# Kernel optimization log

Hardware: AMD Instinct MI355X
Metric: run time of the kernel (lower is better)

The kernel has to match this reference:

```python
import jax, jax.numpy as jnp
import numpy as np

B, S, F, DV, H, DH, L = 32, 600, 9, 1024, 16, 64, 2


def setup_inputs() -> dict:
    key = jax.random.key(0)
    ks = jax.random.split(key, 24)
    w = lambda k, shape, s=0.05: jax.random.normal(k, shape, dtype=jnp.float32) * s
    return {
        "x": w(ks[0], (B, S, F), 1.0),
        "enc_in_W": w(ks[1], (F, DV)), "enc_in_b": w(ks[2], (DV,)),
        "Wq": w(ks[3], (L, H, DV, DH)), "bq": w(ks[4], (L, H, DH)),
        "Wk": w(ks[5], (L, H, DV, DH)), "bk": w(ks[6], (L, H, DH)),
        "Wv": w(ks[7], (L, H, DV, DH)), "bv": w(ks[8], (L, H, DH)),
        "Wo": w(ks[9], (L, DV, DV)), "bo": w(ks[10], (L, DV)),
        "W1": w(ks[11], (L, DV, DV)), "b1": w(ks[12], (L, DV)),
        "W2": w(ks[13], (L, DV, DV)), "b2": w(ks[14], (L, DV)),
        "ln1_w": jnp.ones((L, DV)), "ln1_b": jnp.zeros((L, DV)),
        "ln2_w": jnp.ones((L, DV)), "ln2_b": jnp.zeros((L, DV)),
        "out_W": w(ks[15], (DV, F)), "out_b": w(ks[16], (F,)),
    }


def _layernorm(v, g, b):
    mu = v.mean(-1, keepdims=True)
    var = v.var(-1, keepdims=True)  # biased, matches torch LayerNorm
    return (v - mu) / jnp.sqrt(var + 1e-5) * g + b


def reference(x, enc_in_W, enc_in_b, Wq, bq, Wk, bk, Wv, bv, Wo, bo,
              W1, b1, W2, b2, ln1_w, ln1_b, ln2_w, ln2_b, out_W, out_b):
    # enc_input_fc; pe skipped (code checks pe_mode == 'stardard', never true)
    h = x @ enc_in_W + enc_in_b  # [B,S,DV]
    scale = 1.0 / jnp.sqrt(jnp.float32(DH))
    for l in range(L):
        q = jnp.einsum('bsd,hdk->bhsk', h, Wq[l]) + bq[l][None, :, None, :]
        k = jnp.einsum('bsd,hdk->bhsk', h, Wk[l]) + bk[l][None, :, None, :]
        v = jnp.einsum('bsd,hdk->bhsk', h, Wv[l]) + bv[l][None, :, None, :]
        attn = jax.nn.softmax(jnp.einsum('bhsk,bhtk->bhst', q, k) * scale, axis=-1)
        ctx = jnp.einsum('bhst,bhtk->bhsk', attn, v)  # [B,H,S,DH]
        # torch: stack(heads, dim=-1) -> [B,S,DH,H], then flatten(start_dim=2)
        a = ctx.transpose(0, 2, 3, 1).reshape(B, S, DH * H)
        attn_out = a @ Wo[l] + bo[l]
        x1 = _layernorm(h + attn_out, ln1_w[l], ln1_b[l])
        ff = jax.nn.elu(x1 @ W2[l] + b2[l]) @ W1[l] + b1[l]  # fc1(elu(fc2(x1)))
        h = _layernorm(x1 + ff, ln2_w[l], ln2_b[l])
    out = h @ out_W + out_b  # [B,S,F]; in_seq_len == out_seq_len -> no out_seq_fc
    return out
```

## Files before the change

### kernel.cpp

```cpp
#include <hip/hip_runtime.h>

typedef unsigned short u16;
typedef unsigned int u32;
typedef __attribute__((ext_vector_type(8))) short shortx8;
typedef __attribute__((ext_vector_type(4))) float floatx4;
typedef __attribute__((ext_vector_type(4))) u32 uintx4;
typedef __attribute__((ext_vector_type(2))) u32 uintx2;

#define AS1 __attribute__((address_space(1)))
#define AS3 __attribute__((address_space(3)))

__device__ __forceinline__ float bf2f(u16 u) {
  return __builtin_bit_cast(float, ((u32)u) << 16);
}
__device__ __forceinline__ u16 f2bf(float f) {
  u32 i = __builtin_bit_cast(u32, f);
  u32 r = (i + 0x7fffu + ((i >> 16) & 1u)) >> 16;
  return (u16)r;
}

__launch_bounds__(256)
__global__ void pack_qkv_t(const float* __restrict__ W, u16* __restrict__ dst) {
  __shared__ u16 T[64][72];
  const int kt = blockIdx.x, y = blockIdx.y;
  const int l = y >> 4, h = y & 15;
  const int t = threadIdx.x;
  const int rr = t >> 2, cq = (t & 3) * 16;
  const float* src = W + ((size_t)y * 1024 + kt * 64 + rr) * 64 + cq;
#pragma unroll
  for (int e4 = 0; e4 < 4; ++e4) {
    float4 f = *(const float4*)(src + e4 * 4);
    T[cq + e4 * 4 + 0][rr] = f2bf(f.x);
    T[cq + e4 * 4 + 1][rr] = f2bf(f.y);
    T[cq + e4 * 4 + 2][rr] = f2bf(f.z);
    T[cq + e4 * 4 + 3][rr] = f2bf(f.w);
  }
  __syncthreads();
  const int dd = t >> 2, kq = (t & 3) * 16;
  u16* drow = dst + (size_t)l * 3145728 + ((size_t)h * 64 + dd) * 1024 + kt * 64 + kq;
  *(uintx4*)(drow) = *(const uintx4*)&T[dd][kq];
  *(uintx4*)(drow + 8) = *(const uintx4*)&T[dd][kq + 8];
}

__launch_bounds__(256)
__global__ void pack_sq_t(const float* __restrict__ W, u16* __restrict__ dst) {
  __shared__ u16 T[64][72];
  const int ct = blockIdx.x & 15, rt = blockIdx.x >> 4, l = blockIdx.y;
  const int t = threadIdx.x;
  const int rr = t >> 2, cq = (t & 3) * 16;
  const float* src = W + (size_t)l * 1048576 + (size_t)(rt * 64 + rr) * 1024 + ct * 64 + cq;
#pragma unroll
  for (int e4 = 0; e4 < 4; ++e4) {
    float4 f = *(const float4*)(src + e4 * 4);
    T[cq + e4 * 4 + 0][rr] = f2bf(f.x);
    T[cq + e4 * 4 + 1][rr] = f2bf(f.y);
    T[cq + e4 * 4 + 2][rr] = f2bf(f.z);
    T[cq + e4 * 4 + 3][rr] = f2bf(f.w);
  }
  __syncthreads();
  const int cc = t >> 2, rq = (t & 3) * 16;
  u16* drow = dst + (size_t)l * 1048576 + (size_t)(ct * 64 + cc) * 1024 + rt * 64 + rq;
  *(uintx4*)(drow) = *(const uintx4*)&T[cc][rq];
  *(uintx4*)(drow + 8) = *(const uintx4*)&T[cc][rq + 8];
}

__launch_bounds__(256)
__global__ void pack_wo_t(const float* __restrict__ W, u16* __restrict__ dst) {
  __shared__ u16 T[64][72];
  const int rt = blockIdx.x >> 4, nt = blockIdx.x & 15, l = blockIdx.y;
  const int t = threadIdx.x;
  const int rr = t >> 2, cq = (t & 3) * 16;
  const float* src = W + (size_t)l * 1048576 + (size_t)(rt * 64 + rr) * 1024 + nt * 64 + cq;
#pragma unroll
  for (int e4 = 0; e4 < 4; ++e4) {
    float4 f = *(const float4*)(src + e4 * 4);
    T[cq + e4 * 4 + 0][rr] = f2bf(f.x);
    T[cq + e4 * 4 + 1][rr] = f2bf(f.y);
    T[cq + e4 * 4 + 2][rr] = f2bf(f.z);
    T[cq + e4 * 4 + 3][rr] = f2bf(f.w);
  }
  __syncthreads();
  const int hh = t & 15;
#pragma unroll
  for (int pass = 0; pass < 4; ++pass) {
    const int nl = pass * 16 + (t >> 4);
    uintx2 pk;
    u16 v0 = T[nl][0 * 16 + hh], v1 = T[nl][1 * 16 + hh];
    u16 v2 = T[nl][2 * 16 + hh], v3 = T[nl][3 * 16 + hh];
    pk[0] = (u32)v0 | ((u32)v1 << 16);
    pk[1] = (u32)v2 | ((u32)v3 << 16);
    *(uintx2*)&dst[(size_t)l * 1048576 + (size_t)(nt * 64 + nl) * 1024 + hh * 64 + rt * 4] = pk;
  }
}

__launch_bounds__(256)
__global__ void pack_bias(const float* __restrict__ bq, const float* __restrict__ bk,
                          const float* __restrict__ bv, float* __restrict__ bias) {
  const int i = blockIdx.x * 256 + threadIdx.x;
  const int l = i / 3072, n = i % 3072;
  const int which = n >> 10, nn = n & 1023;
  const float* s = (which == 0) ? bq : (which == 1) ? bk : bv;
  bias[i] = s[l * 1024 + nn];
}

__launch_bounds__(256)
__global__ void enc_kernel(const float* __restrict__ x, const float* __restrict__ W,
                           const float* __restrict__ bias, u16* __restrict__ h) {
  const size_t i = (size_t)blockIdx.x * 256 + threadIdx.x;
  const int m = (int)(i >> 10), n = (int)(i & 1023);
  const float* xr = x + (size_t)m * 9;
  float acc = bias[n];
#pragma unroll
  for (int f = 0; f < 9; ++f) acc += xr[f] * W[f * 1024 + n];
  h[i] = f2bf(acc);
}

template <int EPI>
__launch_bounds__(256)
__global__ void gemm_bt(const u16* __restrict__ A, int lda,
                        const u16* __restrict__ Bt,
                        const float* __restrict__ bias,
                        const u16* __restrict__ R, int ldr,
                        u16* __restrict__ C, int ldc) {
  constexpr int K = 1024;
  __shared__ u16 As[128 * 64];
  __shared__ u16 Bs[128 * 64];
  const int tid = threadIdx.x;
  const int lane = tid & 63;
  const int w = tid >> 6;
  const int wr = w >> 1, wc = w & 1;
  const int m0 = blockIdx.y * 128, n0 = blockIdx.x * 128;

  floatx4 acc[4][4];
#pragma unroll
  for (int i = 0; i < 4; ++i)
#pragma unroll
    for (int j = 0; j < 4; ++j) acc[i][j] = (floatx4){0.f, 0.f, 0.f, 0.f};

  const u16* Ab = A + (size_t)m0 * lda;
  const u16* Bb = Bt + (size_t)n0 * K;

  for (int k0 = 0; k0 < K; k0 += 64) {
#pragma unroll
    for (int p = 0; p < 4; ++p) {
      const int o = p * 4096 + tid * 16;
      const int row = o >> 7;
      const int ke = (o & 127) >> 1;
      __builtin_amdgcn_global_load_lds((const AS1 void*)(Ab + (size_t)row * lda + (k0 + ke)),
                                       (AS3 void*)((char*)As + o), 16, 0, 0);
      __builtin_amdgcn_global_load_lds((const AS1 void*)(Bb + (size_t)row * K + (k0 + ke)),
                                       (AS3 void*)((char*)Bs + o), 16, 0, 0);
    }
    __syncthreads();
#pragma unroll
    for (int ks = 0; ks < 2; ++ks) {
      shortx8 af[4], bfr[4];
#pragma unroll
      for (int i = 0; i < 4; ++i) {
        const int ar = wr * 64 + i * 16 + (lane & 15);
        af[i] = *(const shortx8*)&As[ar * 64 + ks * 32 + (lane >> 4) * 8];
        const int br = wc * 64 + i * 16 + (lane & 15);
        bfr[i] = *(const shortx8*)&Bs[br * 64 + ks * 32 + (lane >> 4) * 8];
      }
#pragma unroll
      for (int i = 0; i < 4; ++i)
#pragma unroll
        for (int j = 0; j < 4; ++j)
          acc[i][j] = __builtin_amdgcn_mfma_f32_16x16x32_bf16(af[i], bfr[j], acc[i][j], 0, 0, 0);
    }
    __syncthreads();
  }

  const int lr = (lane >> 4) * 4, lc = lane & 15;
#pragma unroll
  for (int i = 0; i < 4; ++i) {
#pragma unroll
    for (int j = 0; j < 4; ++j) {
      const int col = n0 + wc * 64 + j * 16 + lc;
      const float bv = bias[col];
#pragma unroll
      for (int r = 0; r < 4; ++r) {
        const int row = m0 + wr * 64 + i * 16 + lr + r;
        float v = acc[i][j][r] + bv;
        if (EPI == 1) v += bf2f(R[(size_t)row * ldr + col]);
        if (EPI == 2) v = v > 0.f ? v : expm1f(v);
        C[(size_t)row * ldc + col] = f2bf(v);
      }
    }
  }
}

__launch_bounds__(512)
__global__ void gemm_bt_wide(const u16* __restrict__ A, int lda,
                             const u16* __restrict__ Bt,
                             const float* __restrict__ bias,
                             u16* __restrict__ C, int ldc) {
  constexpr int K = 1024;
  __shared__ u16 As[128 * 64];
  __shared__ u16 Bs[256 * 64];
  const int tid = threadIdx.x;
  const int lane = tid & 63;
  const int w = tid >> 6;
  const int wr = w >> 2, wc = w & 3;
  const int m0 = blockIdx.y * 128, n0 = blockIdx.x * 256;

  floatx4 acc[4][4];
#pragma unroll
  for (int i = 0; i < 4; ++i)
#pragma unroll
    for (int j = 0; j < 4; ++j) acc[i][j] = (floatx4){0.f, 0.f, 0.f, 0.f};

  const u16* Ab = A + (size_t)m0 * lda;
  const u16* Bb = Bt + (size_t)n0 * K;

  for (int k0 = 0; k0 < K; k0 += 64) {
#pragma unroll
    for (int p = 0; p < 2; ++p) {
      const int o = p * 8192 + tid * 16;
      const int row = o >> 7;
      const int ke = (o & 127) >> 1;
      __builtin_amdgcn_global_load_lds((const AS1 void*)(Ab + (size_t)row * lda + (k0 + ke)),
                                       (AS3 void*)((char*)As + o), 16, 0, 0);
    }
#pragma unroll
    for (int p = 0; p < 4; ++p) {
      const int o = p * 8192 + tid * 16;
      const int row = o >> 7;
      const int ke = (o & 127) >> 1;
      __builtin_amdgcn_global_load_lds((const AS1 void*)(Bb + (size_t)row * K + (k0 + ke)),
                                       (AS3 void*)((char*)Bs + o), 16, 0, 0);
    }
    __syncthreads();
#pragma unroll
    for (int ks = 0; ks < 2; ++ks) {
      shortx8 af[4], bfr[4];
#pragma unroll
      for (int i = 0; i < 4; ++i) {
        const int ar = wr * 64 + i * 16 + (lane & 15);
        af[i] = *(const shortx8*)&As[ar * 64 + ks * 32 + (lane >> 4) * 8];
        const int br = wc * 64 + i * 16 + (lane & 15);
        bfr[i] = *(const shortx8*)&Bs[br * 64 + ks * 32 + (lane >> 4) * 8];
      }
#pragma unroll
      for (int i = 0; i < 4; ++i)
#pragma unroll
        for (int j = 0; j < 4; ++j)
          acc[i][j] = __builtin_amdgcn_mfma_f32_16x16x32_bf16(af[i], bfr[j], acc[i][j], 0, 0, 0);
    }
    __syncthreads();
  }

  const int lr = (lane >> 4) * 4, lc = lane & 15;
#pragma unroll
  for (int i = 0; i < 4; ++i) {
#pragma unroll
    for (int j = 0; j < 4; ++j) {
      const int col = n0 + wc * 64 + j * 16 + lc;
      const float bv = bias[col];
#pragma unroll
      for (int r = 0; r < 4; ++r) {
        const int row = m0 + wr * 64 + i * 16 + lr + r;
        C[(size_t)row * ldc + col] = f2bf(acc[i][j][r] + bv);
      }
    }
  }
}

__launch_bounds__(256)
__global__ void attn_mfma(const u16* __restrict__ qkv, u16* __restrict__ aout) {
  const int qt = blockIdx.x, bh = blockIdx.y;
  const int b = bh >> 4, h = bh & 15;
  const int tid = threadIdx.x, lane = tid & 63, w = tid >> 6;
  const int g = lane >> 4, lq = lane & 15;

  __shared__ u16 K_ld[128 * 72];
  __shared__ u16 Vt[64 * 136];
  __shared__ u16 P_ld[4][16 * 136];

  const size_t bbase = (size_t)b * 600 * 3072;
  const int q0 = qt * 128 + w * 32;

  shortx8 aq[2][2];
#pragma unroll
  for (int sub = 0; sub < 2; ++sub) {
    const int s = q0 + sub * 16 + lq;
    if (s < 600) {
      const u16* qp = qkv + bbase + (size_t)s * 3072 + h * 64 + g * 8;
      aq[sub][0] = *(const shortx8*)qp;
      aq[sub][1] = *(const shortx8*)(qp + 32);
    } else {
      aq[sub][0] = (shortx8){0, 0, 0, 0, 0, 0, 0, 0};
      aq[sub][1] = (shortx8){0, 0, 0, 0, 0, 0, 0, 0};
    }
  }

  floatx4 Oa[2][4];
  float m[2][4], l[2][4];
#pragma unroll
  for (int sub = 0; sub < 2; ++sub) {
#pragma unroll
    for (int db = 0; db < 4; ++db) Oa[sub][db] = (floatx4){0.f, 0.f, 0.f, 0.f};
#pragma unroll
    for (int r = 0; r < 4; ++r) { m[sub][r] = -1e30f; l[sub][r] = 0.f; }
  }

  for (int ch = 0; ch < 5; ++ch) {
    const int t0 = ch * 128;
    __syncthreads();
    {
      const int tloc = tid >> 1, dhalf = (tid & 1) * 32;
      const int tg = t0 + tloc;
      if (tg < 600) {
        const u16* kp = qkv + bbase + (size_t)tg * 3072 + 1024 + h * 64 + dhalf;
        const u16* vp = kp + 1024;
#pragma unroll
        for (int c = 0; c < 4; ++c)
          *(uintx4*)&K_ld[tloc * 72 + dhalf + c * 8] = *(const uintx4*)(kp + c * 8);
#pragma unroll
        for (int c = 0; c < 4; ++c) {
          shortx8 vv = *(const shortx8*)(vp + c * 8);
#pragma unroll
          for (int e = 0; e < 8; ++e)
            Vt[(dhalf + c * 8 + e) * 136 + tloc] = (u16)vv[e];
        }
      } else {
        const uintx4 z4 = (uintx4){0, 0, 0, 0};
#pragma unroll
        for (int c = 0; c < 4; ++c)
          *(uintx4*)&K_ld[tloc * 72 + dhalf + c * 8] = z4;
#pragma unroll
        for (int c = 0; c < 4; ++c)
#pragma unroll
          for (int e = 0; e < 8; ++e)
            Vt[(dhalf + c * 8 + e) * 136 + tloc] = 0;
      }
    }
    __syncthreads();

#pragma unroll
    for (int sub = 0; sub < 2; ++sub) {
      floatx4 S[8];
#pragma unroll
      for (int jb = 0; jb < 8; ++jb) {
        S[jb] = (floatx4){0.f, 0.f, 0.f, 0.f};
#pragma unroll
        for (int ks = 0; ks < 2; ++ks) {
          shortx8 bk = *(const shortx8*)&K_ld[(jb * 16 + lq) * 72 + ks * 32 + g * 8];
          S[jb] = __builtin_amdgcn_mfma_f32_16x16x32_bf16(aq[sub][ks], bk, S[jb], 0, 0, 0);
        }
      }
#pragma unroll
      for (int jb = 0; jb < 8; ++jb) {
        const int tg = t0 + jb * 16 + lq;
        const bool ok = tg < 600;
#pragma unroll
        for (int r = 0; r < 4; ++r) S[jb][r] = ok ? S[jb][r] * 0.125f : -1e30f;
      }

      float scale[4];
#pragma unroll
      for (int r = 0; r < 4; ++r) {
        float v = S[0][r];
#pragma unroll
        for (int jb = 1; jb < 8; ++jb) v = fmaxf(v, S[jb][r]);
        v = fmaxf(v, __shfl_xor(v, 1));
        v = fmaxf(v, __shfl_xor(v, 2));
        v = fmaxf(v, __shfl_xor(v, 4));
        v = fmaxf(v, __shfl_xor(v, 8));
        const float mn = fmaxf(m[sub][r], v);
        scale[r] = __expf(m[sub][r] - mn);
        m[sub][r] = mn;
        l[sub][r] *= scale[r];
      }
#pragma unroll
      for (int db = 0; db < 4; ++db)
#pragma unroll
        for (int r = 0; r < 4; ++r) Oa[sub][db][r] *= scale[r];

      float sums[4] = {0.f, 0.f, 0.f, 0.f};
#pragma unroll
      for (int jb = 0; jb < 8; ++jb)
#pragma unroll
        for (int r = 0; r < 4; ++r) {
          const float p = __expf(S[jb][r] - m[sub][r]);
          sums[r] += p;
          P_ld[w][(g * 4 + r) * 136 + jb * 16 + lq] = f2bf(p);
        }
#pragma unroll
      for (int r = 0; r < 4; ++r) {
        float v = sums[r];
        v += __shfl_xor(v, 1);
        v += __shfl_xor(v, 2);
        v += __shfl_xor(v, 4);
        v += __shfl_xor(v, 8);
        l[sub][r] += v;
      }

#pragma unroll
      for (int ks = 0; ks < 4; ++ks) {
        shortx8 ap = *(const shortx8*)&P_ld[w][lq * 136 + ks * 32 + g * 8];
#pragma unroll
        for (int db = 0; db < 4; ++db) {
          shortx8 bv = *(const shortx8*)&Vt[(db * 16 + lq) * 136 + ks * 32 + g * 8];
          Oa[sub][db] = __builtin_amdgcn_mfma_f32_16x16x32_bf16(ap, bv, Oa[sub][db], 0, 0, 0);
        }
      }
    }
  }

#pragma unroll
  for (int sub = 0; sub < 2; ++sub) {
#pragma unroll
    for (int r = 0; r < 4; ++r) {
      const int sg = q0 + sub * 16 + g * 4 + r;
      if (sg < 600) {
        const float inv = 1.f / l[sub][r];
        u16* orow = aout + ((size_t)(b * 600 + sg)) * 1024 + h * 64;
#pragma unroll
        for (int db = 0; db < 4; ++db)
          orow[db * 16 + lq] = f2bf(Oa[sub][db][r] * inv);
      }
    }
  }
}

__launch_bounds__(256)
__global__ void ln_kernel(const u16* __restrict__ y, int ldy,
                          const float* __restrict__ g, const float* __restrict__ be,
                          u16* __restrict__ o, int ldo) {
  const int row = blockIdx.x, tid = threadIdx.x;
  const int lane = tid & 63, wv = tid >> 6;
  const u16* yr = y + (size_t)row * ldy;
  const int c = tid * 4;
  const uintx2 yv = *(const uintx2*)&yr[c];
  float v0 = bf2f((u16)(yv[0] & 0xffffu)), v1 = bf2f((u16)(yv[0] >> 16));
  float v2 = bf2f((u16)(yv[1] & 0xffffu)), v3 = bf2f((u16)(yv[1] >> 16));
  float s = v0 + v1 + v2 + v3;
  float q = v0 * v0 + v1 * v1 + v2 * v2 + v3 * v3;
#pragma unroll
  for (int m = 32; m; m >>= 1) {
    s += __shfl_xor(s, m);
    q += __shfl_xor(q, m);
  }
  __shared__ float red[2][4];
  if (lane == 0) {
    red[0][wv] = s;
    red[1][wv] = q;
  }
  __syncthreads();
  s = red[0][0] + red[0][1] + red[0][2] + red[0][3];
  q = red[1][0] + red[1][1] + red[1][2] + red[1][3];
  const float mu = s * (1.f / 1024.f);
  const float var = q * (1.f / 1024.f) - mu * mu;
  const float rstd = rsqrtf(var + 1e-5f);
  const float4 gv = *(const float4*)&g[c];
  const float4 bev = *(const float4*)&be[c];
  const float o0 = (v0 - mu) * rstd * gv.x + bev.x;
  const float o1 = (v1 - mu) * rstd * gv.y + bev.y;
  const float o2 = (v2 - mu) * rstd * gv.z + bev.z;
  const float o3 = (v3 - mu) * rstd * gv.w + bev.w;
  uintx2 ov;
  ov[0] = (u32)f2bf(o0) | ((u32)f2bf(o1) << 16);
  ov[1] = (u32)f2bf(o2) | ((u32)f2bf(o3) << 16);
  *(uintx2*)&o[(size_t)row * ldo + c] = ov;
}

__launch_bounds__(256)
__global__ void out_kernel(const u16* __restrict__ h, const float* __restrict__ W,
                           const float* __restrict__ bias, float* __restrict__ out) {
  const int m = blockIdx.x * 4 + (threadIdx.x >> 6);
  const int lane = threadIdx.x & 63;
  float acc[9];
#pragma unroll
  for (int f = 0; f < 9; ++f) acc[f] = 0.f;
  const u16* hr = h + (size_t)m * 1024;
#pragma unroll 4
  for (int j = 0; j < 16; ++j) {
    const int k = lane + j * 64;
    const float hv = bf2f(hr[k]);
    const float* wr = W + (size_t)k * 9;
#pragma unroll
    for (int f = 0; f < 9; ++f) acc[f] += hv * wr[f];
  }
#pragma unroll
  for (int f = 0; f < 9; ++f)
#pragma unroll
    for (int mm = 32; mm; mm >>= 1) acc[f] += __shfl_xor(acc[f], mm);
  if (lane < 9) out[(size_t)m * 9 + lane] = acc[lane] + bias[lane];
}

extern "C" void kernel_launch(void* const* d_in, const int* in_sizes, int n_in,
                              void* d_out, int out_size, void* d_ws, size_t ws_size,
                              hipStream_t stream) {
  (void)in_sizes; (void)n_in; (void)out_size; (void)ws_size;
  const float* x     = (const float*)d_in[0];
  const float* encW  = (const float*)d_in[1];
  const float* encB  = (const float*)d_in[2];
  const float* Wq    = (const float*)d_in[3];
  const float* bq    = (const float*)d_in[4];
  const float* Wk    = (const float*)d_in[5];
  const float* bk    = (const float*)d_in[6];
  const float* Wv    = (const float*)d_in[7];
  const float* bv    = (const float*)d_in[8];
  const float* Wo    = (const float*)d_in[9];
  const float* bo    = (const float*)d_in[10];
  const float* W1    = (const float*)d_in[11];
  const float* b1    = (const float*)d_in[12];
  const float* W2    = (const float*)d_in[13];
  const float* b2    = (const float*)d_in[14];
  const float* ln1w  = (const float*)d_in[15];
  const float* ln1b  = (const float*)d_in[16];
  const float* ln2w  = (const float*)d_in[17];
  const float* ln2b  = (const float*)d_in[18];
  const float* outW  = (const float*)d_in[19];
  const float* outB  = (const float*)d_in[20];
  float* out = (float*)d_out;

  char* ws = (char*)d_ws;
  size_t off = 0;
  auto alloc = [&](size_t bytes) -> void* {
    void* p = ws + off;
    off += (bytes + 255) & ~(size_t)255;
    return p;
  };
  u16* h    = (u16*)alloc(19660800ull * 2);
  u16* qkv  = (u16*)alloc(58982400ull * 2);
  u16* abuf = (u16*)alloc(19660800ull * 2);
  u16* Bqkv = (u16*)alloc(6291456ull * 2);
  u16* Bwo  = (u16*)alloc(2097152ull * 2);
  u16* Bw1  = (u16*)alloc(2097152ull * 2);
  u16* Bw2  = (u16*)alloc(2097152ull * 2);
  float* bqkv = (float*)alloc(6144ull * 4);
  u16* ybuf = qkv;
  u16* x1   = qkv + 1024;
  u16* mid  = qkv + 2048;
  u16* y2   = abuf;

  pack_qkv_t<<<dim3(16, 32), 256, 0, stream>>>(Wq, Bqkv);
  pack_qkv_t<<<dim3(16, 32), 256, 0, stream>>>(Wk, Bqkv + 1048576);
  pack_qkv_t<<<dim3(16, 32), 256, 0, stream>>>(Wv, Bqkv + 2097152);
  pack_wo_t<<<dim3(256, 2), 256, 0, stream>>>(Wo, Bwo);
  pack_sq_t<<<dim3(256, 2), 256, 0, stream>>>(W1, Bw1);
  pack_sq_t<<<dim3(256, 2), 256, 0, stream>>>(W2, Bw2);
  pack_bias<<<24, 256, 0, stream>>>(bq, bk, bv, bqkv);
  enc_kernel<<<76800, 256, 0, stream>>>(x, encW, encB, h);

  for (int l = 0; l < 2; ++l) {
    gemm_bt_wide<<<dim3(12, 150), 512, 0, stream>>>(
        h, 1024, Bqkv + (size_t)l * 3145728, bqkv + l * 3072, qkv, 3072);
    attn_mfma<<<dim3(5, 512), 256, 0, stream>>>(qkv, abuf);
    gemm_bt<1><<<dim3(8, 150), 256, 0, stream>>>(
        abuf, 1024, Bwo + (size_t)l * 1048576, bo + l * 1024, h, 1024, ybuf, 3072);
    ln_kernel<<<19200, 256, 0, stream>>>(ybuf, 3072, ln1w + l * 1024, ln1b + l * 1024, x1, 3072);
    gemm_bt<2><<<dim3(8, 150), 256, 0, stream>>>(
        x1, 3072, Bw2 + (size_t)l * 1048576, b2 + l * 1024, nullptr, 0, mid, 3072);
    gemm_bt<1><<<dim3(8, 150), 256, 0, stream>>>(
        mid, 3072, Bw1 + (size_t)l * 1048576, b1 + l * 1024, x1, 3072, y2, 1024);
    ln_kernel<<<19200, 256, 0, stream>>>(y2, 1024, ln2w + l * 1024, ln2b + l * 1024, h, 1024);
  }
  out_kernel<<<4800, 256, 0, stream>>>(h, outW, outB, out);
}
```

Before: 1.288 ms.

## Use wide 128x256 GEMM for all projections and lazily rescale attention softmax

Templates the wide 128x256 GEMM on its epilogue (residual add, ELU) and routes the output projection and both FFN GEMMs through it, removing the 128x128 kernel. This increases B-tile reuse per block but halves the number of blocks. The attention kernel now applies the sequence mask only on the last key chunk and skips the online-softmax rescale unless the row max grows by more than a threshold. It also raises wave priority around the MFMA sections. The lazy rescale lets unnormalised probabilities grow up to e^8, with some risk to bf16 precision.

```diff
diff --git a/kernel.cpp b/kernel.cpp
--- a/kernel.cpp
+++ b/kernel.cpp
@@ -116,84 +116,11 @@
 }
 
 template <int EPI>
-__launch_bounds__(256)
-__global__ void gemm_bt(const u16* __restrict__ A, int lda,
-                        const u16* __restrict__ Bt,
-                        const float* __restrict__ bias,
-                        const u16* __restrict__ R, int ldr,
-                        u16* __restrict__ C, int ldc) {
-  constexpr int K = 1024;
-  __shared__ u16 As[128 * 64];
-  __shared__ u16 Bs[128 * 64];
-  const int tid = threadIdx.x;
-  const int lane = tid & 63;
-  const int w = tid >> 6;
-  const int wr = w >> 1, wc = w & 1;
-  const int m0 = blockIdx.y * 128, n0 = blockIdx.x * 128;
-
-  floatx4 acc[4][4];
-#pragma unroll
-  for (int i = 0; i < 4; ++i)
-#pragma unroll
-    for (int j = 0; j < 4; ++j) acc[i][j] = (floatx4){0.f, 0.f, 0.f, 0.f};
-
-  const u16* Ab = A + (size_t)m0 * lda;
-  const u16* Bb = Bt + (size_t)n0 * K;
-
-  for (int k0 = 0; k0 < K; k0 += 64) {
-#pragma unroll
-    for (int p = 0; p < 4; ++p) {
-      const int o = p * 4096 + tid * 16;
-      const int row = o >> 7;
-      const int ke = (o & 127) >> 1;
-      __builtin_amdgcn_global_load_lds((const AS1 void*)(Ab + (size_t)row * lda + (k0 + ke)),
-                                       (AS3 void*)((char*)As + o), 16, 0, 0);
-      __builtin_amdgcn_global_load_lds((const AS1 void*)(Bb + (size_t)row * K + (k0 + ke)),
-                                       (AS3 void*)((char*)Bs + o), 16, 0, 0);
-    }
-    __syncthreads();
-#pragma unroll
-    for (int ks = 0; ks < 2; ++ks) {
-      shortx8 af[4], bfr[4];
-#pragma unroll
-      for (int i = 0; i < 4; ++i) {
-        const int ar = wr * 64 + i * 16 + (lane & 15);
-        af[i] = *(const shortx8*)&As[ar * 64 + ks * 32 + (lane >> 4) * 8];
-        const int br = wc * 64 + i * 16 + (lane & 15);
-        bfr[i] = *(const shortx8*)&Bs[br * 64 + ks * 32 + (lane >> 4) * 8];
-      }
-#pragma unroll
-      for (int i = 0; i < 4; ++i)
-#pragma unroll
-        for (int j = 0; j < 4; ++j)
-          acc[i][j] = __builtin_amdgcn_mfma_f32_16x16x32_bf16(af[i], bfr[j], acc[i][j], 0, 0, 0);
-    }
-    __syncthreads();
-  }
-
-  const int lr = (lane >> 4) * 4, lc = lane & 15;
-#pragma unroll
-  for (int i = 0; i < 4; ++i) {
-#pragma unroll
-    for (int j = 0; j < 4; ++j) {
-      const int col = n0 + wc * 64 + j * 16 + lc;
-      const float bv = bias[col];
-#pragma unroll
-      for (int r = 0; r < 4; ++r) {
-        const int row = m0 + wr * 64 + i * 16 + lr + r;
-        float v = acc[i][j][r] + bv;
-        if (EPI == 1) v += bf2f(R[(size_t)row * ldr + col]);
-        if (EPI == 2) v = v > 0.f ? v : expm1f(v);
-        C[(size_t)row * ldc + col] = f2bf(v);
-      }
-    }
-  }
-}
-
 __launch_bounds__(512)
 __global__ void gemm_bt_wide(const u16* __restrict__ A, int lda,
                              const u16* __restrict__ Bt,
                              const float* __restrict__ bias,
+                             const u16* __restrict__ R, int ldr,
                              u16* __restrict__ C, int ldc) {
   constexpr int K = 1024;
   __shared__ u16 As[128 * 64];
@@ -260,7 +187,10 @@
 #pragma unroll
       for (int r = 0; r < 4; ++r) {
         const int row = m0 + wr * 64 + i * 16 + lr + r;
-        C[(size_t)row * ldc + col] = f2bf(acc[i][j][r] + bv);
+        float v = acc[i][j][r] + bv;
+        if (EPI == 1) v += bf2f(R[(size_t)row * ldr + col]);
+        if (EPI == 2) v = v > 0.f ? v : expm1f(v);
+        C[(size_t)row * ldc + col] = f2bf(v);
       }
     }
   }
@@ -340,6 +270,7 @@
 #pragma unroll
     for (int sub = 0; sub < 2; ++sub) {
       floatx4 S[8];
+      __builtin_amdgcn_s_setprio(1);
 #pragma unroll
       for (int jb = 0; jb < 8; ++jb) {
         S[jb] = (floatx4){0.f, 0.f, 0.f, 0.f};
@@ -349,15 +280,23 @@
           S[jb] = __builtin_amdgcn_mfma_f32_16x16x32_bf16(aq[sub][ks], bk, S[jb], 0, 0, 0);
         }
       }
-#pragma unroll
-      for (int jb = 0; jb < 8; ++jb) {
-        const int tg = t0 + jb * 16 + lq;
-        const bool ok = tg < 600;
-#pragma unroll
-        for (int r = 0; r < 4; ++r) S[jb][r] = ok ? S[jb][r] * 0.125f : -1e30f;
-      }
-
-      float scale[4];
+      __builtin_amdgcn_s_setprio(0);
+      if (ch == 4) {
+#pragma unroll
+        for (int jb = 0; jb < 8; ++jb) {
+          const bool ok = (t0 + jb * 16 + lq) < 600;
+#pragma unroll
+          for (int r = 0; r < 4; ++r) S[jb][r] = ok ? S[jb][r] * 0.125f : -1e30f;
+        }
+      } else {
+#pragma unroll
+        for (int jb = 0; jb < 8; ++jb)
+#pragma unroll
+          for (int r = 0; r < 4; ++r) S[jb][r] *= 0.125f;
+      }
+
+      float vmax[4];
+      bool need = false;
 #pragma unroll
       for (int r = 0; r < 4; ++r) {
         float v = S[0][r];
@@ -367,15 +306,20 @@
         v = fmaxf(v, __shfl_xor(v, 2));
         v = fmaxf(v, __shfl_xor(v, 4));
         v = fmaxf(v, __shfl_xor(v, 8));
-        const float mn = fmaxf(m[sub][r], v);
-        scale[r] = __expf(m[sub][r] - mn);
-        m[sub][r] = mn;
-        l[sub][r] *= scale[r];
-      }
-#pragma unroll
-      for (int db = 0; db < 4; ++db)
-#pragma unroll
-        for (int r = 0; r < 4; ++r) Oa[sub][db][r] *= scale[r];
+        vmax[r] = v;
+        need |= (v > m[sub][r] + 8.0f);
+      }
+      if (__any(need ? 1 : 0)) {
+#pragma unroll
+        for (int r = 0; r < 4; ++r) {
+          const float mn = fmaxf(m[sub][r], vmax[r]);
+          const float sc = __expf(m[sub][r] - mn);
+          m[sub][r] = mn;
+          l[sub][r] *= sc;
+#pragma unroll
+          for (int db = 0; db < 4; ++db) Oa[sub][db][r] *= sc;
+        }
+      }
 
       float sums[4] = {0.f, 0.f, 0.f, 0.f};
 #pragma unroll
@@ -396,6 +340,7 @@
         l[sub][r] += v;
       }
 
+      __builtin_amdgcn_s_setprio(1);
 #pragma unroll
       for (int ks = 0; ks < 4; ++ks) {
         shortx8 ap = *(const shortx8*)&P_ld[w][lq * 136 + ks * 32 + g * 8];
@@ -405,6 +350,7 @@
           Oa[sub][db] = __builtin_amdgcn_mfma_f32_16x16x32_bf16(ap, bv, Oa[sub][db], 0, 0, 0);
         }
       }
+      __builtin_amdgcn_s_setprio(0);
     }
   }
 
@@ -546,15 +492,15 @@
   enc_kernel<<<76800, 256, 0, stream>>>(x, encW, encB, h);
 
   for (int l = 0; l < 2; ++l) {
-    gemm_bt_wide<<<dim3(12, 150), 512, 0, stream>>>(
-        h, 1024, Bqkv + (size_t)l * 3145728, bqkv + l * 3072, qkv, 3072);
+    gemm_bt_wide<0><<<dim3(12, 150), 512, 0, stream>>>(
+        h, 1024, Bqkv + (size_t)l * 3145728, bqkv + l * 3072, nullptr, 0, qkv, 3072);
     attn_mfma<<<dim3(5, 512), 256, 0, stream>>>(qkv, abuf);
-    gemm_bt<1><<<dim3(8, 150), 256, 0, stream>>>(
+    gemm_bt_wide<1><<<dim3(4, 150), 512, 0, stream>>>(
         abuf, 1024, Bwo + (size_t)l * 1048576, bo + l * 1024, h, 1024, ybuf, 3072);
     ln_kernel<<<19200, 256, 0, stream>>>(ybuf, 3072, ln1w + l * 1024, ln1b + l * 1024, x1, 3072);
-    gemm_bt<2><<<dim3(8, 150), 256, 0, stream>>>(
+    gemm_bt_wide<2><<<dim3(4, 150), 512, 0, stream>>>(
         x1, 3072, Bw2 + (size_t)l * 1048576, b2 + l * 1024, nullptr, 0, mid, 3072);
-    gemm_bt<1><<<dim3(8, 150), 256, 0, stream>>>(
+    gemm_bt_wide<1><<<dim3(4, 150), 512, 0, stream>>>(
         mid, 3072, Bw1 + (size_t)l * 1048576, b1 + l * 1024, x1, 3072, y2, 1024);
     ln_kernel<<<19200, 256, 0, stream>>>(y2, 1024, ln2w + l * 1024, ln2b + l * 1024, h, 1024);
   }
```

Result: faster. 1.254 ms (-2.6%).
